# Optimization experiments

Hardware: AMD Instinct MI355X
Metric: run time of the kernel (lower is better)

Reference implementation:

```python
import jax, jax.numpy as jnp
import numpy as np

N = 100000   # nodes
E = 1600000  # edges
D = 128      # feature dim (all layer_sizes equal)


def setup_inputs() -> dict:
    key = jax.random.key(0)
    ks = jax.random.split(key, 8)
    s = 1.0 / np.sqrt(D)
    return {
        "x": jax.random.normal(ks[0], (N, D), jnp.float32),
        "edge_index": jax.random.randint(ks[1], (2, E), 0, N, dtype=jnp.int32),
        "W1": jax.random.normal(ks[2], (D, D), jnp.float32) * s,  # GCNConv.lin weight [out,in]
        "b1": jnp.zeros((D,), jnp.float32),
        "a1": jnp.full((1,), 0.25, jnp.float32),  # PReLU slope (torch default)
        "W2": jax.random.normal(ks[3], (D, D), jnp.float32) * s,
        "b2": jnp.zeros((D,), jnp.float32),
        "a2": jnp.full((1,), 0.25, jnp.float32),
    }


def _gcn_conv(x, W, b, row, col, norm):
    # linear transform then normalized scatter-add aggregation
    h = x @ W.T + b                      # [N, D]
    msg = h[row] * norm[:, None]         # [E+N, D] gather + scale
    return jax.ops.segment_sum(msg, col, num_segments=N) # [N, D]


def _prelu(y, a):
    return jnp.where(y > 0, y, a * y)


def reference(x, edge_index, W1, b1, a1, W2, b2, a2):
    src, dst = edge_index[0], edge_index[1]
    loop = jnp.arange(N, dtype=src.dtype)
    # add self loops (GCNConv default add_self_loops=True)
    row = jnp.concatenate([src, loop])
    col = jnp.concatenate([dst, loop])
    # symmetric normalization: deg^{-1/2}[row] * deg^{-1/2}[col]
    deg = jax.ops.segment_sum(jnp.ones_like(col, dtype=x.dtype), col, num_segments=N)
    dis = jnp.where(deg > 0, jax.lax.rsqrt(deg), 0.0)
    norm = dis[row] * dis[col]
    # layer 1: GCNConv -> Identity (batchnorm=False) -> PReLU
    h = _prelu(_gcn_conv(x, W1, b1, row, col, norm), a1)
    # layer 2
    h = _prelu(_gcn_conv(h, W2, b2, row, col, norm), a2)
    return h
```

## Files before the change

kernel.cpp:

```cpp
#include <hip/hip_runtime.h>
#include <hip/hip_fp16.h>

#define D 128
#define PCH 2048

typedef _Float16 half_t;
typedef _Float16 f16x8 __attribute__((ext_vector_type(8)));
typedef _Float16 f16x4 __attribute__((ext_vector_type(4)));
typedef float    f32x4 __attribute__((ext_vector_type(4)));


__global__ __launch_bounds__(256) void k_hist(const int* __restrict__ dstv, int* bcnt,
                                              int e, int nb) {
    __shared__ int h[512];
    for (int i = threadIdx.x; i < nb; i += 256) h[i] = 0;
    __syncthreads();
    int stride = gridDim.x * 256;
    for (int i = blockIdx.x * 256 + threadIdx.x; i < e; i += stride)
        atomicAdd(&h[dstv[i] >> 8], 1);
    __syncthreads();
    for (int i = threadIdx.x; i < nb; i += 256)
        if (h[i]) atomicAdd(&bcnt[i], h[i]);
}

__global__ __launch_bounds__(512) void k_bscan(const int* __restrict__ bcnt, int* bbase,
                                               int* bcur, int nb, int e) {
    __shared__ int sd[512];
    int t = threadIdx.x;
    int v = (t < nb) ? bcnt[t] : 0;
    sd[t] = v;
    __syncthreads();
    for (int off = 1; off < 512; off <<= 1) {
        int x = (t >= off) ? sd[t - off] : 0;
        __syncthreads();
        sd[t] += x;
        __syncthreads();
    }
    int excl = sd[t] - v;
    if (t < nb) { bbase[t] = excl; bcur[t] = excl; }
    if (t == nb - 1) bbase[nb] = e;
}

__global__ __launch_bounds__(256) void k_part(const int* __restrict__ srcv,
                                              const int* __restrict__ dstv,
                                              int* bcur, unsigned int* __restrict__ ebuf,
                                              int e, int nb) {
    __shared__ int h[512];
    __shared__ int base[512];
    int c0 = blockIdx.x * PCH;
    int c1 = min(c0 + PCH, e);
    for (int i = threadIdx.x; i < nb; i += 256) h[i] = 0;
    __syncthreads();
    for (int i = c0 + threadIdx.x; i < c1; i += 256)
        atomicAdd(&h[dstv[i] >> 8], 1);
    __syncthreads();
    for (int i = threadIdx.x; i < nb; i += 256) {
        int c = h[i];
        base[i] = c ? atomicAdd(&bcur[i], c) : 0;
    }
    __syncthreads();
    for (int i = threadIdx.x; i < nb; i += 256) h[i] = 0;
    __syncthreads();
    for (int i = c0 + threadIdx.x; i < c1; i += 256) {
        int d = dstv[i];
        int b = d >> 8;
        int pos = atomicAdd(&h[b], 1);
        ebuf[base[b] + pos] = ((unsigned int)srcv[i] << 8) | (unsigned int)(d & 255);
    }
}

__global__ __launch_bounds__(256) void k_bucket(const unsigned int* __restrict__ ebuf,
                                                const int* __restrict__ bbase,
                                                int* __restrict__ rowptr,
                                                int* __restrict__ csr_src,
                                                float* __restrict__ dis, int n, int e) {
    __shared__ int cnt[256];
    __shared__ int off[256];
    int b = blockIdx.x;
    int t = threadIdx.x;
    int s0 = bbase[b], s1 = bbase[b + 1];
    cnt[t] = 0;
    __syncthreads();
    for (int i = s0 + t; i < s1; i += 256)
        atomicAdd(&cnt[ebuf[i] & 255], 1);
    __syncthreads();
    int v = cnt[t];
    off[t] = v;
    __syncthreads();
    for (int o = 1; o < 256; o <<= 1) {
        int x = (t >= o) ? off[t - o] : 0;
        __syncthreads();
        off[t] += x;
        __syncthreads();
    }
    int excl = off[t] - v;
    int node = b * 256 + t;
    if (node < n) {
        rowptr[node] = s0 + excl;
        dis[node] = rsqrtf((float)(v + 1));
    }
    if (b == 0 && t == 0) rowptr[n] = e;
    __syncthreads();
    cnt[t] = excl;
    __syncthreads();
    for (int i = s0 + t; i < s1; i += 256) {
        unsigned int u = ebuf[i];
        int pos = atomicAdd(&cnt[u & 255], 1);
        csr_src[s0 + pos] = (int)(u >> 8);
    }
}

__global__ __launch_bounds__(256) void k_wconv(const float* __restrict__ W1,
                                               const float* __restrict__ W2,
                                               half_t* __restrict__ Wh) {
    int q = blockIdx.x * 256 + threadIdx.x;
    if (q >= 8192) return;
    const float4* src = (q < 4096) ? (const float4*)W1 : (const float4*)W2;
    float4 v = src[q & 4095];
    f16x4 h;
    h[0] = (_Float16)v.x; h[1] = (_Float16)v.y;
    h[2] = (_Float16)v.z; h[3] = (_Float16)v.w;
    ((f16x4*)Wh)[q] = h;
}

template<bool FP16IN>
__global__ __launch_bounds__(512) void k_gemm(const void* __restrict__ Xv,
                                              const half_t* __restrict__ Wh,
                                              const float* __restrict__ B,
                                              const float* __restrict__ dis,
                                              half_t* __restrict__ Gh, int n) {
    __shared__ _Float16 ldsX[128 * 128];
    const int t = threadIdx.x;
    const int row0 = blockIdx.x * 128;

    #pragma unroll
    for (int i = 0; i < 4; ++i) {
        int gid = i * 512 + t;
        int row = gid >> 4, g = gid & 15;
        int grow = row0 + row;
        int so = ((g ^ (row & 7)) * 8);
        f16x8 hv;
        if constexpr (FP16IN) {
            uint4 u = make_uint4(0, 0, 0, 0);
            if (grow < n) u = ((const uint4*)Xv)[(size_t)grow * 16 + g];
            hv = *(f16x8*)&u;
        } else {
            float4 a = make_float4(0.f, 0.f, 0.f, 0.f);
            float4 b = make_float4(0.f, 0.f, 0.f, 0.f);
            if (grow < n) {
                a = ((const float4*)Xv)[(size_t)grow * 32 + g * 2];
                b = ((const float4*)Xv)[(size_t)grow * 32 + g * 2 + 1];
            }
            hv[0] = (_Float16)a.x; hv[1] = (_Float16)a.y;
            hv[2] = (_Float16)a.z; hv[3] = (_Float16)a.w;
            hv[4] = (_Float16)b.x; hv[5] = (_Float16)b.y;
            hv[6] = (_Float16)b.z; hv[7] = (_Float16)b.w;
        }
        *(f16x8*)&ldsX[row * 128 + so] = hv;
    }
    __syncthreads();

    const int w = t >> 6, l = t & 63;
    const int rbase = (w >> 1) * 32;
    const int cbase = (w & 1) * 64;
    const int lr = l & 15, lk = l >> 4;

    f32x4 acc[2][4] = {};

    #pragma unroll
    for (int kb = 0; kb < 4; ++kb) {
        f16x8 bf[4], af[2];
        #pragma unroll
        for (int ct = 0; ct < 4; ++ct) {
            int j = cbase + ct * 16 + lr;
            bf[ct] = *(const f16x8*)(Wh + j * 128 + kb * 32 + lk * 8);
        }
        #pragma unroll
        for (int rt = 0; rt < 2; ++rt) {
            int row = rbase + rt * 16 + lr;
            int G = kb * 4 + lk;
            af[rt] = *(const f16x8*)&ldsX[row * 128 + ((G ^ (row & 7)) * 8)];
        }
        #pragma unroll
        for (int rt = 0; rt < 2; ++rt)
            #pragma unroll
            for (int ct = 0; ct < 4; ++ct)
                acc[rt][ct] = __builtin_amdgcn_mfma_f32_16x16x32_f16(af[rt], bf[ct],
                                                                    acc[rt][ct], 0, 0, 0);
    }

    float bc[4];
    #pragma unroll
    for (int ct = 0; ct < 4; ++ct) bc[ct] = B[cbase + ct * 16 + lr];
    #pragma unroll
    for (int rt = 0; rt < 2; ++rt)
        #pragma unroll
        for (int q = 0; q < 4; ++q) {
            int grow = row0 + rbase + rt * 16 + lk * 4 + q;
            if (grow < n) {
                float ds = dis[grow];
                #pragma unroll
                for (int ct = 0; ct < 4; ++ct) {
                    float v = (acc[rt][ct][q] + bc[ct]) * ds;
                    Gh[(size_t)grow * 128 + cbase + ct * 16 + lr] = (_Float16)v;
                }
            }
        }
}

template<bool FP16OUT>
__global__ __launch_bounds__(256) void k_gather(const half_t* __restrict__ G,
                                                const float* __restrict__ dis,
                                                const int* __restrict__ rowptr,
                                                const int* __restrict__ csr_src,
                                                const float* __restrict__ a,
                                                void* __restrict__ O, int n, int nquad) {
    int wq = (blockIdx.x * 256 + threadIdx.x) >> 6;
    if (wq >= nquad) return;
    int lane = threadIdx.x & 63;
    int node = wq * 4 + (lane >> 4);
    if (node >= n) node = n - 1;
    int sl = lane & 15;

    const uint4* Gv = (const uint4*)G;
    float ac[8];
    {
        uint4 su = Gv[(size_t)node * 16 + sl];
        f16x8 h = *(f16x8*)&su;
        #pragma unroll
        for (int j = 0; j < 8; ++j) ac[j] = (float)h[j];
    }

    int e = rowptr[node], e1 = rowptr[node + 1];
    for (; e + 4 <= e1; e += 4) {
        int s0 = csr_src[e + 0];
        int s1 = csr_src[e + 1];
        int s2 = csr_src[e + 2];
        int s3 = csr_src[e + 3];
        uint4 u0 = Gv[(size_t)s0 * 16 + sl];
        uint4 u1 = Gv[(size_t)s1 * 16 + sl];
        uint4 u2 = Gv[(size_t)s2 * 16 + sl];
        uint4 u3 = Gv[(size_t)s3 * 16 + sl];
        f16x8 h0 = *(f16x8*)&u0;
        f16x8 h1 = *(f16x8*)&u1;
        f16x8 h2 = *(f16x8*)&u2;
        f16x8 h3 = *(f16x8*)&u3;
        #pragma unroll
        for (int j = 0; j < 8; ++j)
            ac[j] += (float)h0[j] + (float)h1[j] + (float)h2[j] + (float)h3[j];
    }
    for (; e < e1; ++e) {
        int s = csr_src[e];
        uint4 u = Gv[(size_t)s * 16 + sl];
        f16x8 h = *(f16x8*)&u;
        #pragma unroll
        for (int j = 0; j < 8; ++j) ac[j] += (float)h[j];
    }

    float dsc = dis[node];
    float al = a[0];
    #pragma unroll
    for (int j = 0; j < 8; ++j) {
        float v = ac[j] * dsc;
        ac[j] = v > 0.f ? v : al * v;
    }
    if constexpr (FP16OUT) {
        f16x8 h;
        #pragma unroll
        for (int j = 0; j < 8; ++j) h[j] = (_Float16)ac[j];
        ((f16x8*)O)[(size_t)node * 16 + sl] = h;
    } else {
        float4 o0 = make_float4(ac[0], ac[1], ac[2], ac[3]);
        float4 o1 = make_float4(ac[4], ac[5], ac[6], ac[7]);
        ((float4*)O)[(size_t)node * 32 + sl * 2]     = o0;
        ((float4*)O)[(size_t)node * 32 + sl * 2 + 1] = o1;
    }
}

extern "C" void kernel_launch(void* const* d_in, const int* in_sizes, int n_in,
                              void* d_out, int out_size, void* d_ws, size_t ws_size,
                              hipStream_t stream) {
    const float* x  = (const float*)d_in[0];
    const int*   ei = (const int*)d_in[1];
    const float* W1 = (const float*)d_in[2];
    const float* b1 = (const float*)d_in[3];
    const float* a1 = (const float*)d_in[4];
    const float* W2 = (const float*)d_in[5];
    const float* b2 = (const float*)d_in[6];
    const float* a2 = (const float*)d_in[7];

    const int n = in_sizes[0] / D;
    const int e = in_sizes[1] / 2;
    const int* srcv = ei;
    const int* dstv = ei + e;
    const int nb = (n + 255) >> 8;

    char* ws = (char*)d_ws;
    size_t off = 0;
    auto alloc = [&](size_t bytes) {
        void* p = ws + off;
        off = (off + bytes + 255) & ~(size_t)255;
        return p;
    };
    float*        dis     = (float*)       alloc((size_t)n * 4);
    int*          rowptr  = (int*)         alloc((size_t)(n + 1) * 4);
    int*          csr_src = (int*)         alloc((size_t)e * 4);
    int*          bcnt    = (int*)         alloc(512 * 4);
    int*          bbase   = (int*)         alloc(513 * 4);
    int*          bcur    = (int*)         alloc(512 * 4);
    unsigned int* ebuf    = (unsigned int*)alloc((size_t)e * 4);
    half_t*       bufH    = (half_t*)      alloc((size_t)n * D * 2);
    half_t*       h1h     = (half_t*)      alloc((size_t)n * D * 2);
    half_t*       Wh      = (half_t*)      alloc(2 * 16384 * 2);

    dim3 blk(256);
    const int npart = (e + PCH - 1) / PCH;

    hipMemsetAsync(bcnt, 0, 512 * 4, stream);
    k_wconv <<<32, blk, 0, stream>>>(W1, W2, Wh);
    k_hist  <<<512, blk, 0, stream>>>(dstv, bcnt, e, nb);
    k_bscan <<<1, 512, 0, stream>>>(bcnt, bbase, bcur, nb, e);
    k_part  <<<npart, blk, 0, stream>>>(srcv, dstv, bcur, ebuf, e, nb);
    k_bucket<<<nb, blk, 0, stream>>>(ebuf, bbase, rowptr, csr_src, dis, n, e);

    const int nquad = (n + 3) / 4;
    const int gat_grid = (nquad * 64 + 255) / 256;
    const int gemm_grid = (n + 127) / 128;

    k_gemm<false><<<gemm_grid, 512, 0, stream>>>(x, Wh, b1, dis, bufH, n);
    k_gather<true><<<gat_grid, blk, 0, stream>>>(bufH, dis, rowptr, csr_src, a1, h1h, n, nquad);
    k_gemm<true><<<gemm_grid, 512, 0, stream>>>(h1h, Wh + 16384, b2, dis, bufH, n);
    k_gather<false><<<gat_grid, blk, 0, stream>>>(bufH, dis, rowptr, csr_src, a2, d_out, n, nquad);
}
```

Before: 256.6 us.

## Fuse weight conversion into histogram, stage GEMM output via LDS, widen blocks

Folds the fp32-to-fp16 weight conversion into the histogram kernel as extra blocks, which removes one launch. The partition and bucket kernels move to 512 threads, and the partition chunk size doubles. The GEMM epilogue now writes results into a padded LDS tile and then stores 16-byte vectors per row to global memory, replacing scattered 2-byte stores. This adds an extra sync and LDS traffic, and halves the number of partition blocks, which increases atomic contention per block.

```diff
diff --git a/kernel.cpp b/kernel.cpp
--- a/kernel.cpp
+++ b/kernel.cpp
@@ -2,20 +2,34 @@
 #include <hip/hip_fp16.h>
 
 #define D 128
-#define PCH 2048
+#define PCH 4096
 
 typedef _Float16 half_t;
 typedef _Float16 f16x8 __attribute__((ext_vector_type(8)));
 typedef _Float16 f16x4 __attribute__((ext_vector_type(4)));
 typedef float    f32x4 __attribute__((ext_vector_type(4)));
 
-
-__global__ __launch_bounds__(256) void k_hist(const int* __restrict__ dstv, int* bcnt,
-                                              int e, int nb) {
+__global__ __launch_bounds__(256) void k_histw(const int* __restrict__ dstv, int* bcnt,
+                                               int e, int nb,
+                                               const float* __restrict__ W1,
+                                               const float* __restrict__ W2,
+                                               half_t* __restrict__ Wh) {
+    if (blockIdx.x >= 512) {
+        int q = (blockIdx.x - 512) * 256 + threadIdx.x;
+        if (q < 8192) {
+            const float4* src = (q < 4096) ? (const float4*)W1 : (const float4*)W2;
+            float4 v = src[q & 4095];
+            f16x4 h;
+            h[0] = (_Float16)v.x; h[1] = (_Float16)v.y;
+            h[2] = (_Float16)v.z; h[3] = (_Float16)v.w;
+            ((f16x4*)Wh)[q] = h;
+        }
+        return;
+    }
     __shared__ int h[512];
     for (int i = threadIdx.x; i < nb; i += 256) h[i] = 0;
     __syncthreads();
-    int stride = gridDim.x * 256;
+    const int stride = 512 * 256;
     for (int i = blockIdx.x * 256 + threadIdx.x; i < e; i += stride)
         atomicAdd(&h[dstv[i] >> 8], 1);
     __syncthreads();
@@ -41,7 +55,7 @@
     if (t == nb - 1) bbase[nb] = e;
 }
 
-__global__ __launch_bounds__(256) void k_part(const int* __restrict__ srcv,
+__global__ __launch_bounds__(512) void k_part(const int* __restrict__ srcv,
                                               const int* __restrict__ dstv,
                                               int* bcur, unsigned int* __restrict__ ebuf,
                                               int e, int nb) {
@@ -49,19 +63,19 @@
     __shared__ int base[512];
     int c0 = blockIdx.x * PCH;
     int c1 = min(c0 + PCH, e);
-    for (int i = threadIdx.x; i < nb; i += 256) h[i] = 0;
-    __syncthreads();
-    for (int i = c0 + threadIdx.x; i < c1; i += 256)
+    for (int i = threadIdx.x; i < nb; i += 512) h[i] = 0;
+    __syncthreads();
+    for (int i = c0 + threadIdx.x; i < c1; i += 512)
         atomicAdd(&h[dstv[i] >> 8], 1);
     __syncthreads();
-    for (int i = threadIdx.x; i < nb; i += 256) {
+    for (int i = threadIdx.x; i < nb; i += 512) {
         int c = h[i];
         base[i] = c ? atomicAdd(&bcur[i], c) : 0;
     }
     __syncthreads();
-    for (int i = threadIdx.x; i < nb; i += 256) h[i] = 0;
-    __syncthreads();
-    for (int i = c0 + threadIdx.x; i < c1; i += 256) {
+    for (int i = threadIdx.x; i < nb; i += 512) h[i] = 0;
+    __syncthreads();
+    for (int i = c0 + threadIdx.x; i < c1; i += 512) {
         int d = dstv[i];
         int b = d >> 8;
         int pos = atomicAdd(&h[b], 1);
@@ -69,7 +83,7 @@
     }
 }
 
-__global__ __launch_bounds__(256) void k_bucket(const unsigned int* __restrict__ ebuf,
+__global__ __launch_bounds__(512) void k_bucket(const unsigned int* __restrict__ ebuf,
                                                 const int* __restrict__ bbase,
                                                 int* __restrict__ rowptr,
                                                 int* __restrict__ csr_src,
@@ -79,48 +93,36 @@
     int b = blockIdx.x;
     int t = threadIdx.x;
     int s0 = bbase[b], s1 = bbase[b + 1];
-    cnt[t] = 0;
-    __syncthreads();
-    for (int i = s0 + t; i < s1; i += 256)
+    if (t < 256) cnt[t] = 0;
+    __syncthreads();
+    for (int i = s0 + t; i < s1; i += 512)
         atomicAdd(&cnt[ebuf[i] & 255], 1);
     __syncthreads();
-    int v = cnt[t];
-    off[t] = v;
+    int v = (t < 256) ? cnt[t] : 0;
+    if (t < 256) off[t] = v;
     __syncthreads();
     for (int o = 1; o < 256; o <<= 1) {
-        int x = (t >= o) ? off[t - o] : 0;
+        int x = (t >= o && t < 256) ? off[t - o] : 0;
         __syncthreads();
-        off[t] += x;
+        if (t < 256) off[t] += x;
         __syncthreads();
     }
-    int excl = off[t] - v;
-    int node = b * 256 + t;
-    if (node < n) {
-        rowptr[node] = s0 + excl;
-        dis[node] = rsqrtf((float)(v + 1));
-    }
-    if (b == 0 && t == 0) rowptr[n] = e;
-    __syncthreads();
-    cnt[t] = excl;
-    __syncthreads();
-    for (int i = s0 + t; i < s1; i += 256) {
+    if (t < 256) {
+        int excl = off[t] - v;
+        int node = b * 256 + t;
+        if (node < n) {
+            rowptr[node] = s0 + excl;
+            dis[node] = rsqrtf((float)(v + 1));
+        }
+        if (b == 0 && t == 0) rowptr[n] = e;
+        cnt[t] = excl;
+    }
+    __syncthreads();
+    for (int i = s0 + t; i < s1; i += 512) {
         unsigned int u = ebuf[i];
         int pos = atomicAdd(&cnt[u & 255], 1);
         csr_src[s0 + pos] = (int)(u >> 8);
     }
-}
-
-__global__ __launch_bounds__(256) void k_wconv(const float* __restrict__ W1,
-                                               const float* __restrict__ W2,
-                                               half_t* __restrict__ Wh) {
-    int q = blockIdx.x * 256 + threadIdx.x;
-    if (q >= 8192) return;
-    const float4* src = (q < 4096) ? (const float4*)W1 : (const float4*)W2;
-    float4 v = src[q & 4095];
-    f16x4 h;
-    h[0] = (_Float16)v.x; h[1] = (_Float16)v.y;
-    h[2] = (_Float16)v.z; h[3] = (_Float16)v.w;
-    ((f16x4*)Wh)[q] = h;
 }
 
 template<bool FP16IN>
@@ -129,7 +131,7 @@
                                               const float* __restrict__ B,
                                               const float* __restrict__ dis,
                                               half_t* __restrict__ Gh, int n) {
-    __shared__ _Float16 ldsX[128 * 128];
+    __shared__ _Float16 lds[128 * 136];
     const int t = threadIdx.x;
     const int row0 = blockIdx.x * 128;
 
@@ -156,7 +158,7 @@
             hv[4] = (_Float16)b.x; hv[5] = (_Float16)b.y;
             hv[6] = (_Float16)b.z; hv[7] = (_Float16)b.w;
         }
-        *(f16x8*)&ldsX[row * 128 + so] = hv;
+        *(f16x8*)&lds[row * 128 + so] = hv;
     }
     __syncthreads();
 
@@ -179,7 +181,7 @@
         for (int rt = 0; rt < 2; ++rt) {
             int row = rbase + rt * 16 + lr;
             int G = kb * 4 + lk;
-            af[rt] = *(const f16x8*)&ldsX[row * 128 + ((G ^ (row & 7)) * 8)];
+            af[rt] = *(const f16x8*)&lds[row * 128 + ((G ^ (row & 7)) * 8)];
         }
         #pragma unroll
         for (int rt = 0; rt < 2; ++rt)
@@ -192,20 +194,30 @@
     float bc[4];
     #pragma unroll
     for (int ct = 0; ct < 4; ++ct) bc[ct] = B[cbase + ct * 16 + lr];
+
+    __syncthreads();
     #pragma unroll
     for (int rt = 0; rt < 2; ++rt)
         #pragma unroll
         for (int q = 0; q < 4; ++q) {
-            int grow = row0 + rbase + rt * 16 + lk * 4 + q;
-            if (grow < n) {
-                float ds = dis[grow];
-                #pragma unroll
-                for (int ct = 0; ct < 4; ++ct) {
-                    float v = (acc[rt][ct][q] + bc[ct]) * ds;
-                    Gh[(size_t)grow * 128 + cbase + ct * 16 + lr] = (_Float16)v;
-                }
+            int rl = rbase + rt * 16 + lk * 4 + q;
+            int grow = row0 + rl;
+            float ds = (grow < n) ? dis[grow] : 0.f;
+            #pragma unroll
+            for (int ct = 0; ct < 4; ++ct) {
+                float v = (acc[rt][ct][q] + bc[ct]) * ds;
+                lds[rl * 136 + cbase + ct * 16 + lr] = (_Float16)v;
             }
         }
+    __syncthreads();
+    #pragma unroll
+    for (int i = 0; i < 4; ++i) {
+        int gid = i * 512 + t;
+        int row = gid >> 4, g = gid & 15;
+        int grow = row0 + row;
+        if (grow < n)
+            *(f16x8*)&Gh[(size_t)grow * 128 + g * 8] = *(f16x8*)&lds[row * 136 + g * 8];
+    }
 }
 
 template<bool FP16OUT>
@@ -317,11 +329,10 @@
     const int npart = (e + PCH - 1) / PCH;
 
     hipMemsetAsync(bcnt, 0, 512 * 4, stream);
-    k_wconv <<<32, blk, 0, stream>>>(W1, W2, Wh);
-    k_hist  <<<512, blk, 0, stream>>>(dstv, bcnt, e, nb);
+    k_histw <<<544, blk, 0, stream>>>(dstv, bcnt, e, nb, W1, W2, Wh);
     k_bscan <<<1, 512, 0, stream>>>(bcnt, bbase, bcur, nb, e);
-    k_part  <<<npart, blk, 0, stream>>>(srcv, dstv, bcur, ebuf, e, nb);
-    k_bucket<<<nb, blk, 0, stream>>>(ebuf, bbase, rowptr, csr_src, dis, n, e);
+    k_part  <<<npart, 512, 0, stream>>>(srcv, dstv, bcur, ebuf, e, nb);
+    k_bucket<<<nb, 512, 0, stream>>>(ebuf, bbase, rowptr, csr_src, dis, n, e);
 
     const int nquad = (n + 3) / 4;
     const int gat_grid = (nquad * 64 + 255) / 256;
```

Measured after the change: 237.7 us. -7.4%, faster.
